# Performance work log

Hardware: AMD Instinct MI355X
Metric: run time of the kernel (lower is better)

Reference implementation:

```python
import jax, jax.numpy as jnp
import numpy as np

NUM_NODES = 100_000
NUM_EDGES = 1_200_000
NUM_REL = 3
EMBED_DIM = 64
HIDDEN_DIM = 64
NUM_CLS = 2
NUM_GRAPHS = 512


def setup_inputs() -> dict:
    key = jax.random.key(0)
    ks = jax.random.split(key, 12)
    s = 1.0 / np.sqrt(EMBED_DIM)
    inp = {
        # forward args
        "x": jnp.zeros((NUM_NODES,), dtype=jnp.int64),  # vocab size 1 -> all zeros
        "edge_index": jax.random.randint(ks[0], (2, NUM_EDGES), 0, NUM_NODES, dtype=jnp.int64),
        "edge_type": jax.random.randint(ks[1], (NUM_EDGES,), 0, NUM_REL, dtype=jnp.int64),
        "batch": jnp.sort(jax.random.randint(ks[2], (NUM_NODES,), 0, NUM_GRAPHS, dtype=jnp.int64)),
        # parameters
        "embed_w": jax.random.normal(ks[3], (1, EMBED_DIM), jnp.float32),
        "W1": jax.random.normal(ks[4], (NUM_REL, EMBED_DIM, HIDDEN_DIM), jnp.float32) * s,
        "root1": jax.random.normal(ks[5], (EMBED_DIM, HIDDEN_DIM), jnp.float32) * s,
        "b1": jnp.zeros((HIDDEN_DIM,), jnp.float32),
        "W2": jax.random.normal(ks[6], (NUM_REL, HIDDEN_DIM, HIDDEN_DIM), jnp.float32) * s,
        "root2": jax.random.normal(ks[7], (HIDDEN_DIM, HIDDEN_DIM), jnp.float32) * s,
        "b2": jnp.zeros((HIDDEN_DIM,), jnp.float32),
        "lin_w": jax.random.normal(ks[8], (HIDDEN_DIM, NUM_CLS), jnp.float32) * s,
        "lin_b": jnp.zeros((NUM_CLS,), jnp.float32),
    }
    return inp


def rgcn_conv(h, W, root, b, src, dst, edge_type):
    """PyG RGCNConv with mean aggregation per relation + root weight + bias."""
    n = h.shape[0]
    out = h @ root + b  # root/self contribution, [N, H]
    for r in range(NUM_REL):
        m = (edge_type == r).astype(h.dtype)  # [E]
        tr = h @ W[r]                          # [N, H] small GEMM
        msg = tr[src] * m[:, None]             # gather [E, H]
        ssum = jax.ops.segment_sum(msg, dst, num_segments=n)  # scatter-add [N, H]
        cnt = jax.ops.segment_sum(m, dst, num_segments=n)     # per-relation in-degree
        out = out + ssum / jnp.clip(cnt, 1.0)[:, None]        # mean aggregation
    return out


def reference(x, edge_index, edge_type, batch, embed_w, W1, root1, b1, W2, root2, b2, lin_w, lin_b):
    src, dst = edge_index[0], edge_index[1]
    h = embed_w[x]                                       # [N, D] embedding lookup
    h = jax.nn.relu(rgcn_conv(h, W1, root1, b1, src, dst, edge_type))
    h = jax.nn.relu(rgcn_conv(h, W2, root2, b2, src, dst, edge_type))
    # global mean pool over graphs
    gsum = jax.ops.segment_sum(h, batch, num_segments=NUM_GRAPHS)            # [G, H]
    gcnt = jax.ops.segment_sum(jnp.ones_like(h[:, 0]), batch, num_segments=NUM_GRAPHS)
    g_emb = gsum / jnp.clip(gcnt, 1.0)[:, None]
    return g_emb @ lin_w + lin_b                          # [G, num_cls]
```

## Files before the change

kernel.cpp:

```cpp
#include <hip/hip_runtime.h>

#define NODES   100000
#define EDGES   1200000
#define NREL    3
#define DIM     64
#define NGRAPH  512

#define BSH     8
#define NB      391
#define BUCKCAP 4096
#define SBLK    256
#define CHUNK   4688

#define OFF_GSUM  0
#define OFF_GCNT  131072
#define OFF_CUR   133120
#define OFF_MBN   135168
#define OFF_ZEND  535552
#define OFF_REC   535552
#define OFF_BASE  6941696
#define OFF_T2    6943744

__global__ void k_tab(const float* __restrict__ embed_w, const float* __restrict__ W1,
                      const float* __restrict__ root1, const float* __restrict__ b1,
                      const float* __restrict__ W2, const float* __restrict__ root2,
                      const float* __restrict__ b2,
                      float* __restrict__ base, float* __restrict__ T2,
                      char* __restrict__ ws) {
    {
        uint4* z = (uint4*)ws;
        const uint4 zz = make_uint4(0, 0, 0, 0);
        const int gt = blockIdx.x * 256 + threadIdx.x;
        for (int i = gt; i < OFF_ZEND / 16; i += 32 * 256) z[i] = zz;
    }
    __shared__ float h0[DIM];
    __shared__ float u[DIM];
    __shared__ float t[NREL][DIM];
    __shared__ float h1s[8][DIM];
    __shared__ float red[4][DIM];
    const int tid = threadIdx.x;
    const int j = tid & 63, w = tid >> 6;
    if (tid < DIM) h0[tid] = embed_w[tid];
    __syncthreads();
    {
        const float* M = (w == 0) ? root1 : (W1 + (size_t)(w - 1) * DIM * DIM);
        float s = 0.f;
        for (int k = 0; k < DIM; ++k) s += h0[k] * M[k * DIM + j];
        if (w == 0) u[j] = s + b1[j];
        else        t[w - 1][j] = s;
    }
    __syncthreads();
    for (int p = w; p < 8; p += 4) {
        float v = u[j];
        if (p & 1) v += t[0][j];
        if (p & 2) v += t[1][j];
        if (p & 4) v += t[2][j];
        h1s[p][j] = fmaxf(v, 0.f);
    }
    __syncthreads();
    const int row = blockIdx.x;
    const int p = (row < 8) ? row : ((row - 8) & 7);
    const float* M = (row < 8) ? root2 : (W2 + (size_t)((row - 8) >> 3) * DIM * DIM);
    float s = 0.f;
    for (int k = w * 16; k < w * 16 + 16; ++k) s += h1s[p][k] * M[k * DIM + j];
    red[w][j] = s;
    __syncthreads();
    if (w == 0) {
        const float v = red[0][j] + red[1][j] + red[2][j] + red[3][j];
        if (row < 8) base[p * DIM + j] = v + b2[j];
        else         T2[(row - 8) * DIM + j] = v;
    }
}

__global__ void k_scat(const int* __restrict__ ei, const int* __restrict__ et,
                       int* __restrict__ cursor, unsigned int* __restrict__ rec,
                       unsigned char* __restrict__ mbn) {
    __shared__ int hist[NB];
    __shared__ int cur[NB];
    const int tid = threadIdx.x;
    for (int b = tid; b < NB; b += 256) hist[b] = 0;
    __syncthreads();
    const int e0 = blockIdx.x * CHUNK;
    const int* src = ei;
    const int* dst = ei + EDGES;
    for (int i = tid; i < CHUNK / 4; i += 256) {
        const int e = e0 + i * 4;
        if (e < EDGES) {
            const int4 d4 = *(const int4*)(dst + e);
            atomicAdd(&hist[d4.x >> BSH], 1);
            atomicAdd(&hist[d4.y >> BSH], 1);
            atomicAdd(&hist[d4.z >> BSH], 1);
            atomicAdd(&hist[d4.w >> BSH], 1);
        }
    }
    __syncthreads();
    for (int b = tid; b < NB; b += 256) {
        const int h = hist[b];
        const int r = h ? atomicAdd(&cursor[b], h) : 0;
        cur[b] = b * BUCKCAP + r;
    }
    __syncthreads();
    for (int i = tid; i < CHUNK / 4; i += 256) {
        const int e = e0 + i * 4;
        if (e < EDGES) {
            const int4 s4 = *(const int4*)(src + e);
            const int4 d4 = *(const int4*)(dst + e);
            const int4 r4 = *(const int4*)(et + e);
            int p;
            p = atomicAdd(&cur[d4.x >> BSH], 1);
            if (p < ((d4.x >> BSH) + 1) * BUCKCAP)
                rec[p] = ((unsigned)(d4.x & 255) << 19) | ((unsigned)r4.x << 17) | (unsigned)s4.x;
            mbn[d4.x * 4 + r4.x] = 1;
            p = atomicAdd(&cur[d4.y >> BSH], 1);
            if (p < ((d4.y >> BSH) + 1) * BUCKCAP)
                rec[p] = ((unsigned)(d4.y & 255) << 19) | ((unsigned)r4.y << 17) | (unsigned)s4.y;
            mbn[d4.y * 4 + r4.y] = 1;
            p = atomicAdd(&cur[d4.z >> BSH], 1);
            if (p < ((d4.z >> BSH) + 1) * BUCKCAP)
                rec[p] = ((unsigned)(d4.z & 255) << 19) | ((unsigned)r4.z << 17) | (unsigned)s4.z;
            mbn[d4.z * 4 + r4.z] = 1;
            p = atomicAdd(&cur[d4.w >> BSH], 1);
            if (p < ((d4.w >> BSH) + 1) * BUCKCAP)
                rec[p] = ((unsigned)(d4.w & 255) << 19) | ((unsigned)r4.w << 17) | (unsigned)s4.w;
            mbn[d4.w * 4 + r4.w] = 1;
        }
    }
}

__global__ void k_histnode(const unsigned int* __restrict__ rec,
                           const int* __restrict__ cursor,
                           const unsigned char* __restrict__ mbn,
                           const int* __restrict__ batch,
                           const float* __restrict__ base, const float* __restrict__ T2,
                           float* __restrict__ gsum, int* __restrict__ gcnt) {
    __shared__ unsigned int h[3072];
    __shared__ float bs[8 * DIM];
    __shared__ float ts[24 * DIM];
    const int tid = threadIdx.x;
    const unsigned* mbn32 = (const unsigned*)mbn;
    for (int i = tid; i < 3072; i += 1024) h[i] = 0;
    for (int i = tid; i < 8 * DIM; i += 1024) bs[i] = base[i];
    for (int i = tid; i < 24 * DIM; i += 1024) ts[i] = T2[i];
    __syncthreads();
    const int b = blockIdx.x;
    const int s = b * BUCKCAP;
    int n = cursor[b];
    if (n > BUCKCAP) n = BUCKCAP;
    for (int i = tid; i < n; i += 1024) {
        const unsigned r32 = rec[s + i];
        const unsigned x = mbn32[r32 & 0x1FFFF];
        const int p = (x & 1) | ((x >> 7) & 2) | ((x >> 14) & 4);
        const int idx = (r32 >> 19) * 24 + ((r32 >> 17) & 3) * 8 + p;
        atomicAdd(&h[idx >> 1], 1u << ((idx & 1) * 16));
    }
    __syncthreads();
    const int lane = tid & 63;
    const int w = tid >> 6;
    const int v0 = (b << BSH) + w * 16;
    if (v0 >= NODES) return;
    int pidx = v0 + (lane & 15);
    if (pidx >= NODES) pidx = NODES - 1;
    const int bv = batch[pidx];
    const int mv = (int)mbn32[pidx];
    float acc = 0.f;
    int curg = -1, runlen = 0;
    for (int i = 0; i < 16; ++i) {
        const int v = v0 + i;
        if (v >= NODES) break;
        const int mx = __shfl(mv, i);
        const int pm = (mx & 1) | ((mx >> 7) & 2) | ((mx >> 14) & 4);
        float sacc = bs[pm * DIM + lane];
        const unsigned* hv = &h[(v & 255) * 12];
        #pragma unroll
        for (int r = 0; r < NREL; ++r) {
            const unsigned x0 = hv[r * 4 + 0], x1 = hv[r * 4 + 1];
            const unsigned x2 = hv[r * 4 + 2], x3 = hv[r * 4 + 3];
            const int cr = (int)((x0 & 0xFFFF) + (x0 >> 16) + (x1 & 0xFFFF) + (x1 >> 16)
                               + (x2 & 0xFFFF) + (x2 >> 16) + (x3 & 0xFFFF) + (x3 >> 16));
            if (cr > 0) {
                float msg = 0.f;
                const float* tr = &ts[r * 8 * DIM + lane];
                if (x0) msg += (float)(x0 & 0xFFFF) * tr[0 * DIM]
                             + (float)(x0 >> 16)    * tr[1 * DIM];
                if (x1) msg += (float)(x1 & 0xFFFF) * tr[2 * DIM]
                             + (float)(x1 >> 16)    * tr[3 * DIM];
                if (x2) msg += (float)(x2 & 0xFFFF) * tr[4 * DIM]
                             + (float)(x2 >> 16)    * tr[5 * DIM];
                if (x3) msg += (float)(x3 & 0xFFFF) * tr[6 * DIM]
                             + (float)(x3 >> 16)    * tr[7 * DIM];
                sacc += msg / (float)cr;
            }
        }
        sacc = fmaxf(sacc, 0.f);
        const int g = __shfl(bv, i);
        if (g != curg) {
            if (curg >= 0) {
                atomicAdd(&gsum[curg * DIM + lane], acc);
                if (lane == 0) atomicAdd(&gcnt[curg], runlen);
            }
            curg = g; acc = 0.f; runlen = 0;
        }
        acc += sacc; runlen++;
    }
    if (curg >= 0) {
        atomicAdd(&gsum[curg * DIM + lane], acc);
        if (lane == 0) atomicAdd(&gcnt[curg], runlen);
    }
}

__global__ void k_final(const float* __restrict__ gsum, const int* __restrict__ gcnt,
                        const float* __restrict__ lin_w, const float* __restrict__ lin_b,
                        float* __restrict__ out) {
    const int lane = threadIdx.x & 63;
    const int g = blockIdx.x * (blockDim.x >> 6) + (threadIdx.x >> 6);
    if (g >= NGRAPH) return;
    const float inv = 1.0f / fmaxf((float)gcnt[g], 1.0f);
    const float s = gsum[g * DIM + lane] * inv;
    float p0 = s * lin_w[lane * 2 + 0];
    float p1 = s * lin_w[lane * 2 + 1];
    for (int off = 32; off; off >>= 1) {
        p0 += __shfl_down(p0, off);
        p1 += __shfl_down(p1, off);
    }
    if (lane == 0) {
        out[g * 2 + 0] = p0 + lin_b[0];
        out[g * 2 + 1] = p1 + lin_b[1];
    }
}

extern "C" void kernel_launch(void* const* d_in, const int* in_sizes, int n_in,
                              void* d_out, int out_size, void* d_ws, size_t ws_size,
                              hipStream_t stream) {
    const int*   ei      = (const int*)d_in[1];
    const int*   et      = (const int*)d_in[2];
    const int*   batch   = (const int*)d_in[3];
    const float* embed_w = (const float*)d_in[4];
    const float* W1      = (const float*)d_in[5];
    const float* root1   = (const float*)d_in[6];
    const float* b1      = (const float*)d_in[7];
    const float* W2      = (const float*)d_in[8];
    const float* root2   = (const float*)d_in[9];
    const float* b2      = (const float*)d_in[10];
    const float* lin_w   = (const float*)d_in[11];
    const float* lin_b   = (const float*)d_in[12];
    float* out = (float*)d_out;

    char* ws = (char*)d_ws;
    float*         gsum = (float*)(ws + OFF_GSUM);
    int*           gcnt = (int*)(ws + OFF_GCNT);
    int*           cur  = (int*)(ws + OFF_CUR);
    unsigned char* mbn  = (unsigned char*)(ws + OFF_MBN);
    unsigned int*  rec  = (unsigned int*)(ws + OFF_REC);
    float*         base = (float*)(ws + OFF_BASE);
    float*         T2   = (float*)(ws + OFF_T2);

    k_tab     <<<32,   256,  0, stream>>>(embed_w, W1, root1, b1, W2, root2, b2,
                                          base, T2, ws);
    k_scat    <<<SBLK, 256,  0, stream>>>(ei, et, cur, rec, mbn);
    k_histnode<<<NB,   1024, 0, stream>>>(rec, cur, mbn, batch, base, T2, gsum, gcnt);
    k_final   <<<128,  256,  0, stream>>>(gsum, gcnt, lin_w, lin_b, out);
}
```

Measured before the change: 143.6 us.

## Stage edge records in LDS, split node buckets in halves, fuse final projection

New measurement: 215.1 us. 1.5x slower.

```diff
diff --git a/kernel.cpp b/kernel.cpp
--- a/kernel.cpp
+++ b/kernel.cpp
@@ -8,18 +8,20 @@
 
 #define BSH     8
 #define NB      391
+#define NBN     782
 #define BUCKCAP 4096
 #define SBLK    256
 #define CHUNK   4688
 
-#define OFF_GSUM  0
-#define OFF_GCNT  131072
-#define OFF_CUR   133120
-#define OFF_MBN   135168
-#define OFF_ZEND  535552
-#define OFF_REC   535552
-#define OFF_BASE  6941696
-#define OFF_T2    6943744
+#define OFF_PSUM  0
+#define OFF_PCNT  4096
+#define OFF_CUR   6144
+#define OFF_DONE  8192
+#define OFF_MBN   8256
+#define OFF_ZEND  408256
+#define OFF_REC   408256
+#define OFF_BASE  6814400
+#define OFF_T2    6816448
 
 __global__ void k_tab(const float* __restrict__ embed_w, const float* __restrict__ W1,
                       const float* __restrict__ root1, const float* __restrict__ b1,
@@ -75,6 +77,8 @@
 __global__ void k_scat(const int* __restrict__ ei, const int* __restrict__ et,
                        int* __restrict__ cursor, unsigned int* __restrict__ rec,
                        unsigned char* __restrict__ mbn) {
+    __shared__ unsigned int   srec[CHUNK];
+    __shared__ unsigned short sbkt[CHUNK];
     __shared__ int hist[NB];
     __shared__ int cur[NB];
     const int tid = threadIdx.x;
@@ -86,11 +90,26 @@
     for (int i = tid; i < CHUNK / 4; i += 256) {
         const int e = e0 + i * 4;
         if (e < EDGES) {
+            const int4 s4 = *(const int4*)(src + e);
             const int4 d4 = *(const int4*)(dst + e);
+            const int4 r4 = *(const int4*)(et + e);
+            const int j = i * 4;
+            srec[j + 0] = ((unsigned)(d4.x & 255) << 19) | ((unsigned)r4.x << 17) | (unsigned)s4.x;
+            sbkt[j + 0] = (unsigned short)(d4.x >> BSH);
             atomicAdd(&hist[d4.x >> BSH], 1);
+            mbn[d4.x * 4 + r4.x] = 1;
+            srec[j + 1] = ((unsigned)(d4.y & 255) << 19) | ((unsigned)r4.y << 17) | (unsigned)s4.y;
+            sbkt[j + 1] = (unsigned short)(d4.y >> BSH);
             atomicAdd(&hist[d4.y >> BSH], 1);
+            mbn[d4.y * 4 + r4.y] = 1;
+            srec[j + 2] = ((unsigned)(d4.z & 255) << 19) | ((unsigned)r4.z << 17) | (unsigned)s4.z;
+            sbkt[j + 2] = (unsigned short)(d4.z >> BSH);
             atomicAdd(&hist[d4.z >> BSH], 1);
+            mbn[d4.z * 4 + r4.z] = 1;
+            srec[j + 3] = ((unsigned)(d4.w & 255) << 19) | ((unsigned)r4.w << 17) | (unsigned)s4.w;
+            sbkt[j + 3] = (unsigned short)(d4.w >> BSH);
             atomicAdd(&hist[d4.w >> BSH], 1);
+            mbn[d4.w * 4 + r4.w] = 1;
         }
     }
     __syncthreads();
@@ -100,131 +119,130 @@
         cur[b] = b * BUCKCAP + r;
     }
     __syncthreads();
-    for (int i = tid; i < CHUNK / 4; i += 256) {
-        const int e = e0 + i * 4;
-        if (e < EDGES) {
-            const int4 s4 = *(const int4*)(src + e);
-            const int4 d4 = *(const int4*)(dst + e);
-            const int4 r4 = *(const int4*)(et + e);
-            int p;
-            p = atomicAdd(&cur[d4.x >> BSH], 1);
-            if (p < ((d4.x >> BSH) + 1) * BUCKCAP)
-                rec[p] = ((unsigned)(d4.x & 255) << 19) | ((unsigned)r4.x << 17) | (unsigned)s4.x;
-            mbn[d4.x * 4 + r4.x] = 1;
-            p = atomicAdd(&cur[d4.y >> BSH], 1);
-            if (p < ((d4.y >> BSH) + 1) * BUCKCAP)
-                rec[p] = ((unsigned)(d4.y & 255) << 19) | ((unsigned)r4.y << 17) | (unsigned)s4.y;
-            mbn[d4.y * 4 + r4.y] = 1;
-            p = atomicAdd(&cur[d4.z >> BSH], 1);
-            if (p < ((d4.z >> BSH) + 1) * BUCKCAP)
-                rec[p] = ((unsigned)(d4.z & 255) << 19) | ((unsigned)r4.z << 17) | (unsigned)s4.z;
-            mbn[d4.z * 4 + r4.z] = 1;
-            p = atomicAdd(&cur[d4.w >> BSH], 1);
-            if (p < ((d4.w >> BSH) + 1) * BUCKCAP)
-                rec[p] = ((unsigned)(d4.w & 255) << 19) | ((unsigned)r4.w << 17) | (unsigned)s4.w;
-            mbn[d4.w * 4 + r4.w] = 1;
-        }
-    }
-}
-
-__global__ void k_histnode(const unsigned int* __restrict__ rec,
-                           const int* __restrict__ cursor,
-                           const unsigned char* __restrict__ mbn,
-                           const int* __restrict__ batch,
-                           const float* __restrict__ base, const float* __restrict__ T2,
-                           float* __restrict__ gsum, int* __restrict__ gcnt) {
-    __shared__ unsigned int h[3072];
+    int nl = EDGES - e0;
+    if (nl > CHUNK) nl = CHUNK;
+    for (int i = tid; i < nl; i += 256) {
+        const int b = sbkt[i];
+        const int p = atomicAdd(&cur[b], 1);
+        if (p < (b + 1) * BUCKCAP) rec[p] = srec[i];
+    }
+}
+
+__global__ void k_node(const unsigned int* __restrict__ rec, const int* __restrict__ cursor,
+                       const unsigned char* __restrict__ mbn, const int* __restrict__ batch,
+                       const float* __restrict__ base, const float* __restrict__ T2,
+                       const float* __restrict__ lin_w, const float* __restrict__ lin_b,
+                       float* __restrict__ psum, int* __restrict__ pcnt,
+                       int* __restrict__ done, float* __restrict__ out) {
+    __shared__ unsigned int h[1536];
     __shared__ float bs[8 * DIM];
     __shared__ float ts[24 * DIM];
+    __shared__ int lastflag;
     const int tid = threadIdx.x;
     const unsigned* mbn32 = (const unsigned*)mbn;
-    for (int i = tid; i < 3072; i += 1024) h[i] = 0;
-    for (int i = tid; i < 8 * DIM; i += 1024) bs[i] = base[i];
-    for (int i = tid; i < 24 * DIM; i += 1024) ts[i] = T2[i];
-    __syncthreads();
-    const int b = blockIdx.x;
+    for (int i = tid; i < 1536; i += 512) h[i] = 0;
+    if (tid < 8 * DIM) bs[tid] = base[tid];
+    for (int i = tid; i < 24 * DIM; i += 512) ts[i] = T2[i];
+    __syncthreads();
+    const int bb = blockIdx.x;
+    const int b = bb >> 1, half = bb & 1;
     const int s = b * BUCKCAP;
     int n = cursor[b];
     if (n > BUCKCAP) n = BUCKCAP;
-    for (int i = tid; i < n; i += 1024) {
+    for (int i = tid; i < n; i += 512) {
         const unsigned r32 = rec[s + i];
-        const unsigned x = mbn32[r32 & 0x1FFFF];
-        const int p = (x & 1) | ((x >> 7) & 2) | ((x >> 14) & 4);
-        const int idx = (r32 >> 19) * 24 + ((r32 >> 17) & 3) * 8 + p;
-        atomicAdd(&h[idx >> 1], 1u << ((idx & 1) * 16));
+        if ((int)((r32 >> 26) & 1) == half) {
+            const unsigned x = mbn32[r32 & 0x1FFFF];
+            const int p = (x & 1) | ((x >> 7) & 2) | ((x >> 14) & 4);
+            const int idx = (int)((r32 >> 19) & 127) * 24 + (int)((r32 >> 17) & 3) * 8 + p;
+            atomicAdd(&h[idx >> 1], 1u << ((idx & 1) * 16));
+        }
     }
     __syncthreads();
     const int lane = tid & 63;
     const int w = tid >> 6;
-    const int v0 = (b << BSH) + w * 16;
-    if (v0 >= NODES) return;
-    int pidx = v0 + (lane & 15);
-    if (pidx >= NODES) pidx = NODES - 1;
-    const int bv = batch[pidx];
-    const int mv = (int)mbn32[pidx];
-    float acc = 0.f;
-    int curg = -1, runlen = 0;
-    for (int i = 0; i < 16; ++i) {
-        const int v = v0 + i;
-        if (v >= NODES) break;
-        const int mx = __shfl(mv, i);
-        const int pm = (mx & 1) | ((mx >> 7) & 2) | ((mx >> 14) & 4);
-        float sacc = bs[pm * DIM + lane];
-        const unsigned* hv = &h[(v & 255) * 12];
-        #pragma unroll
-        for (int r = 0; r < NREL; ++r) {
-            const unsigned x0 = hv[r * 4 + 0], x1 = hv[r * 4 + 1];
-            const unsigned x2 = hv[r * 4 + 2], x3 = hv[r * 4 + 3];
-            const int cr = (int)((x0 & 0xFFFF) + (x0 >> 16) + (x1 & 0xFFFF) + (x1 >> 16)
-                               + (x2 & 0xFFFF) + (x2 >> 16) + (x3 & 0xFFFF) + (x3 >> 16));
-            if (cr > 0) {
-                float msg = 0.f;
-                const float* tr = &ts[r * 8 * DIM + lane];
-                if (x0) msg += (float)(x0 & 0xFFFF) * tr[0 * DIM]
-                             + (float)(x0 >> 16)    * tr[1 * DIM];
-                if (x1) msg += (float)(x1 & 0xFFFF) * tr[2 * DIM]
-                             + (float)(x1 >> 16)    * tr[3 * DIM];
-                if (x2) msg += (float)(x2 & 0xFFFF) * tr[4 * DIM]
-                             + (float)(x2 >> 16)    * tr[5 * DIM];
-                if (x3) msg += (float)(x3 & 0xFFFF) * tr[6 * DIM]
-                             + (float)(x3 >> 16)    * tr[7 * DIM];
-                sacc += msg / (float)cr;
-            }
-        }
-        sacc = fmaxf(sacc, 0.f);
-        const int g = __shfl(bv, i);
-        if (g != curg) {
-            if (curg >= 0) {
-                atomicAdd(&gsum[curg * DIM + lane], acc);
-                if (lane == 0) atomicAdd(&gcnt[curg], runlen);
-            }
-            curg = g; acc = 0.f; runlen = 0;
-        }
-        acc += sacc; runlen++;
-    }
-    if (curg >= 0) {
-        atomicAdd(&gsum[curg * DIM + lane], acc);
-        if (lane == 0) atomicAdd(&gcnt[curg], runlen);
-    }
-}
-
-__global__ void k_final(const float* __restrict__ gsum, const int* __restrict__ gcnt,
-                        const float* __restrict__ lin_w, const float* __restrict__ lin_b,
-                        float* __restrict__ out) {
-    const int lane = threadIdx.x & 63;
-    const int g = blockIdx.x * (blockDim.x >> 6) + (threadIdx.x >> 6);
-    if (g >= NGRAPH) return;
-    const float inv = 1.0f / fmaxf((float)gcnt[g], 1.0f);
-    const float s = gsum[g * DIM + lane] * inv;
-    float p0 = s * lin_w[lane * 2 + 0];
-    float p1 = s * lin_w[lane * 2 + 1];
-    for (int off = 32; off; off >>= 1) {
-        p0 += __shfl_down(p0, off);
-        p1 += __shfl_down(p1, off);
-    }
-    if (lane == 0) {
-        out[g * 2 + 0] = p0 + lin_b[0];
-        out[g * 2 + 1] = p1 + lin_b[1];
+    const int v0 = (b << 8) + half * 128 + w * 16;
+    const float lw0 = lin_w[lane * 2 + 0];
+    const float lw1 = lin_w[lane * 2 + 1];
+    if (v0 < NODES) {
+        int pidx = v0 + (lane & 15);
+        if (pidx >= NODES) pidx = NODES - 1;
+        const int bv = batch[pidx];
+        const int mv = (int)mbn32[pidx];
+        float acc = 0.f;
+        int curg = -1, runlen = 0;
+        for (int i = 0; i < 16; ++i) {
+            const int v = v0 + i;
+            if (v >= NODES) break;
+            const int mx = __shfl(mv, i);
+            const int pm = (mx & 1) | ((mx >> 7) & 2) | ((mx >> 14) & 4);
+            float sacc = bs[pm * DIM + lane];
+            const unsigned* hv = &h[(w * 16 + i) * 12];
+            #pragma unroll
+            for (int r = 0; r < NREL; ++r) {
+                const unsigned x0 = hv[r * 4 + 0], x1 = hv[r * 4 + 1];
+                const unsigned x2 = hv[r * 4 + 2], x3 = hv[r * 4 + 3];
+                const int cr = (int)((x0 & 0xFFFF) + (x0 >> 16) + (x1 & 0xFFFF) + (x1 >> 16)
+                                   + (x2 & 0xFFFF) + (x2 >> 16) + (x3 & 0xFFFF) + (x3 >> 16));
+                if (cr > 0) {
+                    float msg = 0.f;
+                    const float* tr = &ts[r * 8 * DIM + lane];
+                    if (x0) msg += (float)(x0 & 0xFFFF) * tr[0 * DIM]
+                                 + (float)(x0 >> 16)    * tr[1 * DIM];
+                    if (x1) msg += (float)(x1 & 0xFFFF) * tr[2 * DIM]
+                                 + (float)(x1 >> 16)    * tr[3 * DIM];
+                    if (x2) msg += (float)(x2 & 0xFFFF) * tr[4 * DIM]
+                                 + (float)(x2 >> 16)    * tr[5 * DIM];
+                    if (x3) msg += (float)(x3 & 0xFFFF) * tr[6 * DIM]
+                                 + (float)(x3 >> 16)    * tr[7 * DIM];
+                    sacc += msg / (float)cr;
+                }
+            }
+            sacc = fmaxf(sacc, 0.f);
+            const int g = __shfl(bv, i);
+            if (g != curg) {
+                if (curg >= 0) {
+                    float p0 = acc * lw0, p1 = acc * lw1;
+                    #pragma unroll
+                    for (int off = 32; off; off >>= 1) {
+                        p0 += __shfl_down(p0, off);
+                        p1 += __shfl_down(p1, off);
+                    }
+                    if (lane == 0) {
+                        atomicAdd(&psum[curg * 2 + 0], p0);
+                        atomicAdd(&psum[curg * 2 + 1], p1);
+                        atomicAdd(&pcnt[curg], runlen);
+                    }
+                }
+                curg = g; acc = 0.f; runlen = 0;
+            }
+            acc += sacc; runlen++;
+        }
+        if (curg >= 0) {
+            float p0 = acc * lw0, p1 = acc * lw1;
+            #pragma unroll
+            for (int off = 32; off; off >>= 1) {
+                p0 += __shfl_down(p0, off);
+                p1 += __shfl_down(p1, off);
+            }
+            if (lane == 0) {
+                atomicAdd(&psum[curg * 2 + 0], p0);
+                atomicAdd(&psum[curg * 2 + 1], p1);
+                atomicAdd(&pcnt[curg], runlen);
+            }
+        }
+    }
+    __threadfence();
+    __syncthreads();
+    if (tid == 0) lastflag = (atomicAdd(done, 1) == NBN - 1) ? 1 : 0;
+    __syncthreads();
+    if (lastflag && tid < NGRAPH) {
+        const float q0 = atomicAdd(&psum[tid * 2 + 0], 0.0f);
+        const float q1 = atomicAdd(&psum[tid * 2 + 1], 0.0f);
+        const int   c  = atomicAdd(&pcnt[tid], 0);
+        const float inv = 1.0f / fmaxf((float)c, 1.0f);
+        out[tid * 2 + 0] = q0 * inv + lin_b[0];
+        out[tid * 2 + 1] = q1 * inv + lin_b[1];
     }
 }
 
@@ -246,17 +264,18 @@
     float* out = (float*)d_out;
 
     char* ws = (char*)d_ws;
-    float*         gsum = (float*)(ws + OFF_GSUM);
-    int*           gcnt = (int*)(ws + OFF_GCNT);
+    float*         psum = (float*)(ws + OFF_PSUM);
+    int*           pcnt = (int*)(ws + OFF_PCNT);
     int*           cur  = (int*)(ws + OFF_CUR);
+    int*           done = (int*)(ws + OFF_DONE);
     unsigned char* mbn  = (unsigned char*)(ws + OFF_MBN);
     unsigned int*  rec  = (unsigned int*)(ws + OFF_REC);
     float*         base = (float*)(ws + OFF_BASE);
     float*         T2   = (float*)(ws + OFF_T2);
 
-    k_tab     <<<32,   256,  0, stream>>>(embed_w, W1, root1, b1, W2, root2, b2,
-                                          base, T2, ws);
-    k_scat    <<<SBLK, 256,  0, stream>>>(ei, et, cur, rec, mbn);
-    k_histnode<<<NB,   1024, 0, stream>>>(rec, cur, mbn, batch, base, T2, gsum, gcnt);
-    k_final   <<<128,  256,  0, stream>>>(gsum, gcnt, lin_w, lin_b, out);
-}
+    k_tab <<<32,   256, 0, stream>>>(embed_w, W1, root1, b1, W2, root2, b2,
+                                     base, T2, (char*)d_ws);
+    k_scat<<<SBLK, 256, 0, stream>>>(ei, et, cur, rec, mbn);
+    k_node<<<NBN,  512, 0, stream>>>(rec, cur, mbn, batch, base, T2, lin_w, lin_b,
+                                     psum, pcnt, done, out);
+}
```
